# Kernel optimization log

Hardware: AMD Instinct MI355X
Metric: run time of the kernel (lower is better)

## Reference

```python
import jax, jax.numpy as jnp
import numpy as np

WAY = 5  # N_way from init


def setup_inputs() -> dict:
    key = jax.random.key(0)
    k1, k2, k3, k4 = jax.random.split(key, 4)
    N, c, h, w = 80, 2048, 16, 16
    S = 512  # shuffle_num
    x = jax.random.normal(k1, (N, c, h, w), dtype=jnp.float32)
    s_ca = jax.random.uniform(k2, (N, c, 1, 1), dtype=jnp.float32)
    # random channel indices per sample (stand-in for random.sample)
    rand_index = jax.random.randint(k3, (N, S), 0, c)
    # partner offset per sample (stand-in for random j != i)
    partner = jax.random.randint(k4, (N,), 0, N - 1)
    return {"x": x, "s_ca": s_ca, "rand_index": rand_index,
            "partner": partner, "shuffle_num": S}


def reference(x, s_ca, rand_index, partner, shuffle_num):
    N, c, h, w = x.shape
    way = WAY
    scores = s_ca.reshape(N, c)
    # per-sample top-k channels by attention score
    _, topk_idx = jax.lax.top_k(scores, shuffle_num)          # [N, S]
    # partner sample j != i (offset trick guarantees inequality)
    j = (jnp.arange(N) + 1 + partner) % N                      # [N]
    bi = jnp.arange(N)[:, None]                                # [N, 1]
    x_topk = x[bi, topk_idx]                                   # [N, S, h, w]
    x_part = x[j[:, None], rand_index]                         # [N, S, h, w]
    blend = 0.7 * x_topk + 0.3 * x_part
    # scatter blended channels back (batched gather-blend-scatter)
    aug_x = x.at[bi, topk_idx].set(blend)                      # [N, c, h, w]
    # group into (way, shot, ...) and concat original + augmented episodes
    x_r = x.reshape(way, -1, c, h, w)
    aug_r = aug_x.reshape(way, -1, c, h, w)
    out = jnp.concatenate((x_r, aug_r), axis=1)                # [way, 2*shot, c, h, w]
    s = s_ca.reshape(way, -1, c, 1, 1)
    s = jnp.concatenate((s, s), axis=1)                        # repeat(1,2,1,1,1)
    out = out * s
    return out.reshape(-1, c, h, w)                            # [2N, c, h, w]
```

## Files before the change

kernel.cpp:

```cpp
#include <hip/hip_runtime.h>

#define N_SAMP 80
#define C_CH   2048
#define HW     256
#define S_TOP  512
#define HW4    64

__global__ __launch_bounds__(256) void topk_rank_kernel(
    const float* __restrict__ s_ca, int* __restrict__ rank) {
  __shared__ unsigned long long keys[C_CH];
  const int n = blockIdx.x;
  const int tid = threadIdx.x;
  const float* row = s_ca + (size_t)n * C_CH;

  for (int i = tid; i < C_CH; i += 256) {
    unsigned int b = __float_as_uint(row[i]);
    b ^= (b & 0x80000000u) ? 0xFFFFFFFFu : 0x80000000u;
    keys[i] = ((unsigned long long)b << 11) |
              (unsigned long long)(C_CH - 1 - i);
  }
  __syncthreads();

  for (int k = 2; k <= C_CH; k <<= 1) {
    for (int j = k >> 1; j > 0; j >>= 1) {
      for (int t = tid; t < C_CH / 2; t += 256) {
        int i = ((t & ~(j - 1)) << 1) | (t & (j - 1));
        int ixj = i | j;
        bool desc = ((i & k) == 0);
        unsigned long long a = keys[i];
        unsigned long long c2 = keys[ixj];
        if ((a < c2) == desc) {
          keys[i] = c2;
          keys[ixj] = a;
        }
      }
      __syncthreads();
    }
  }

  int* rrow = rank + (size_t)n * C_CH;
  for (int i = tid; i < C_CH; i += 256) rrow[i] = -1;
  __syncthreads();
  for (int t = tid; t < S_TOP; t += 256) {
    int idx = (C_CH - 1) - (int)(keys[t] & 2047ULL);
    rrow[idx] = t;
  }
}

__global__ __launch_bounds__(256) void shuffle_out_kernel(
    const float4* __restrict__ x4, const float* __restrict__ s_ca,
    const int* __restrict__ rand_index, const int* __restrict__ partner,
    const int* __restrict__ rank, float4* __restrict__ out4) {
  const unsigned int p = blockIdx.x * 256u + threadIdx.x;
  const unsigned int m = p >> 17;
  const unsigned int r = p & 131071u;
  const unsigned int ch = r >> 6;
  const unsigned int q = r & 63u;

  const unsigned int b = m & 31u;
  const unsigned int n = ((m >> 5) << 4) | (b & 15u);
  const bool aug = (b >= 16u);

  const float s = s_ca[(size_t)n * C_CH + ch];
  float4 v = x4[((size_t)n * C_CH + ch) * HW4 + q];

  if (aug) {
    const int k = rank[(size_t)n * C_CH + ch];
    if (k >= 0) {
      int jn = (int)n + 1 + partner[n];
      if (jn >= N_SAMP) jn -= N_SAMP;
      const int pc = rand_index[(size_t)n * S_TOP + k];
      const float4 u = x4[((size_t)jn * C_CH + pc) * HW4 + q];
      v.x = 0.7f * v.x + 0.3f * u.x;
      v.y = 0.7f * v.y + 0.3f * u.y;
      v.z = 0.7f * v.z + 0.3f * u.z;
      v.w = 0.7f * v.w + 0.3f * u.w;
    }
  }

  v.x *= s; v.y *= s; v.z *= s; v.w *= s;
  out4[p] = v;
}

extern "C" void kernel_launch(void* const* d_in, const int* in_sizes, int n_in,
                              void* d_out, int out_size, void* d_ws,
                              size_t ws_size, hipStream_t stream) {
  const float* x = (const float*)d_in[0];
  const float* s_ca = (const float*)d_in[1];
  const int* rand_index = (const int*)d_in[2];
  const int* partner = (const int*)d_in[3];

  int* rank = (int*)d_ws;

  topk_rank_kernel<<<N_SAMP, 256, 0, stream>>>(s_ca, rank);

  const int nblocks = (2 * N_SAMP * C_CH * HW4) / 256;
  shuffle_out_kernel<<<nblocks, 256, 0, stream>>>(
      (const float4*)x, s_ca, rand_index, partner, rank, (float4*)d_out);
}
```

Before: 498.9 us.

## Replace bitonic top-k with rank counting and fuse plain/aug output writes

Swaps the single-block-per-sample bitonic sort for a rank-by-counting kernel that launches 8 blocks per sample, with each thread comparing its key against all 2048 keys in the row. This removes the barrier-heavy, low-occupancy sort. The output kernel now handles each input channel once per wave and writes both the plain and the augmented copies, so x is read once instead of twice. Stores are marked nontemporal. The trade-off is O(C^2) comparisons per sample, served from cached global loads.

```diff
diff --git a/kernel.cpp b/kernel.cpp
--- a/kernel.cpp
+++ b/kernel.cpp
@@ -6,80 +6,67 @@
 #define S_TOP  512
 #define HW4    64
 
-__global__ __launch_bounds__(256) void topk_rank_kernel(
+typedef float vfloat4 __attribute__((ext_vector_type(4)));
+
+__global__ __launch_bounds__(256) void rank_count_kernel(
     const float* __restrict__ s_ca, int* __restrict__ rank) {
-  __shared__ unsigned long long keys[C_CH];
-  const int n = blockIdx.x;
-  const int tid = threadIdx.x;
-  const float* row = s_ca + (size_t)n * C_CH;
+  const int n = blockIdx.x >> 3;
+  const int i = ((blockIdx.x & 7) << 8) | threadIdx.x;
+  const float* __restrict__ row = s_ca + (size_t)n * C_CH;
 
-  for (int i = tid; i < C_CH; i += 256) {
-    unsigned int b = __float_as_uint(row[i]);
-    b ^= (b & 0x80000000u) ? 0xFFFFFFFFu : 0x80000000u;
-    keys[i] = ((unsigned long long)b << 11) |
-              (unsigned long long)(C_CH - 1 - i);
+  unsigned int bi = __float_as_uint(row[i]);
+  bi ^= (bi & 0x80000000u) ? 0xFFFFFFFFu : 0x80000000u;
+  const unsigned long long ki =
+      ((unsigned long long)bi << 11) | (unsigned long long)(C_CH - 1 - i);
+
+  int cnt = 0;
+#pragma unroll 8
+  for (int j = 0; j < C_CH; ++j) {
+    unsigned int bj = __float_as_uint(row[j]);
+    bj ^= (bj & 0x80000000u) ? 0xFFFFFFFFu : 0x80000000u;
+    const unsigned long long kj =
+        ((unsigned long long)bj << 11) | (unsigned long long)(C_CH - 1 - j);
+    cnt += (kj > ki) ? 1 : 0;
   }
-  __syncthreads();
-
-  for (int k = 2; k <= C_CH; k <<= 1) {
-    for (int j = k >> 1; j > 0; j >>= 1) {
-      for (int t = tid; t < C_CH / 2; t += 256) {
-        int i = ((t & ~(j - 1)) << 1) | (t & (j - 1));
-        int ixj = i | j;
-        bool desc = ((i & k) == 0);
-        unsigned long long a = keys[i];
-        unsigned long long c2 = keys[ixj];
-        if ((a < c2) == desc) {
-          keys[i] = c2;
-          keys[ixj] = a;
-        }
-      }
-      __syncthreads();
-    }
-  }
-
-  int* rrow = rank + (size_t)n * C_CH;
-  for (int i = tid; i < C_CH; i += 256) rrow[i] = -1;
-  __syncthreads();
-  for (int t = tid; t < S_TOP; t += 256) {
-    int idx = (C_CH - 1) - (int)(keys[t] & 2047ULL);
-    rrow[idx] = t;
-  }
+  rank[(size_t)n * C_CH + i] = (cnt < S_TOP) ? cnt : -1;
 }
 
-__global__ __launch_bounds__(256) void shuffle_out_kernel(
+__global__ __launch_bounds__(256) void shuffle_out_fused(
     const float4* __restrict__ x4, const float* __restrict__ s_ca,
     const int* __restrict__ rand_index, const int* __restrict__ partner,
     const int* __restrict__ rank, float4* __restrict__ out4) {
-  const unsigned int p = blockIdx.x * 256u + threadIdx.x;
-  const unsigned int m = p >> 17;
-  const unsigned int r = p & 131071u;
-  const unsigned int ch = r >> 6;
-  const unsigned int q = r & 63u;
+  const unsigned int lane = threadIdx.x & 63u;
+  const unsigned int pw = blockIdx.x * 4u + (threadIdx.x >> 6);
+  const unsigned int n = pw >> 11;
+  const unsigned int ch = pw & 2047u;
+  const unsigned int g = n >> 4;
+  const unsigned int b = n & 15u;
 
-  const unsigned int b = m & 31u;
-  const unsigned int n = ((m >> 5) << 4) | (b & 15u);
-  const bool aug = (b >= 16u);
+  const size_t out_plain =
+      (((size_t)((g << 5) | b) * C_CH + ch) << 6) | lane;
+  const size_t out_aug = out_plain + ((size_t)(16 * C_CH) << 6);
 
-  const float s = s_ca[(size_t)n * C_CH + ch];
-  float4 v = x4[((size_t)n * C_CH + ch) * HW4 + q];
+  const float s = s_ca[pw];
+  const float4 v = x4[((size_t)pw << 6) | lane];
+  float4 pv = make_float4(v.x * s, v.y * s, v.z * s, v.w * s);
+  float4 av = pv;
 
-  if (aug) {
-    const int k = rank[(size_t)n * C_CH + ch];
-    if (k >= 0) {
-      int jn = (int)n + 1 + partner[n];
-      if (jn >= N_SAMP) jn -= N_SAMP;
-      const int pc = rand_index[(size_t)n * S_TOP + k];
-      const float4 u = x4[((size_t)jn * C_CH + pc) * HW4 + q];
-      v.x = 0.7f * v.x + 0.3f * u.x;
-      v.y = 0.7f * v.y + 0.3f * u.y;
-      v.z = 0.7f * v.z + 0.3f * u.z;
-      v.w = 0.7f * v.w + 0.3f * u.w;
-    }
+  const int k = rank[pw];
+  if (k >= 0) {
+    int jn = (int)n + 1 + partner[n];
+    if (jn >= N_SAMP) jn -= N_SAMP;
+    const int pc = rand_index[(size_t)n * S_TOP + k];
+    const float4 u = x4[((((size_t)jn << 11) | (size_t)pc) << 6) | lane];
+    av.x = (0.7f * v.x + 0.3f * u.x) * s;
+    av.y = (0.7f * v.y + 0.3f * u.y) * s;
+    av.z = (0.7f * v.z + 0.3f * u.z) * s;
+    av.w = (0.7f * v.w + 0.3f * u.w) * s;
   }
 
-  v.x *= s; v.y *= s; v.z *= s; v.w *= s;
-  out4[p] = v;
+  __builtin_nontemporal_store(*(const vfloat4*)&pv,
+                              (vfloat4*)&out4[out_plain]);
+  __builtin_nontemporal_store(*(const vfloat4*)&av,
+                              (vfloat4*)&out4[out_aug]);
 }
 
 extern "C" void kernel_launch(void* const* d_in, const int* in_sizes, int n_in,
@@ -92,9 +79,9 @@
 
   int* rank = (int*)d_ws;
 
-  topk_rank_kernel<<<N_SAMP, 256, 0, stream>>>(s_ca, rank);
+  rank_count_kernel<<<N_SAMP * 8, 256, 0, stream>>>(s_ca, rank);
 
-  const int nblocks = (2 * N_SAMP * C_CH * HW4) / 256;
-  shuffle_out_kernel<<<nblocks, 256, 0, stream>>>(
+  const int nblocks = (N_SAMP * C_CH) / 4;
+  shuffle_out_fused<<<nblocks, 256, 0, stream>>>(
       (const float4*)x, s_ca, rand_index, partner, rank, (float4*)d_out);
 }
```

Measured after the change: 561.5 us. +12.6%, slower.
